# Performance work log

Measured on AMD Instinct MI355X. Metric: run time of the kernel, lower is better.

## Reference

```python
import jax, jax.numpy as jnp
import numpy as np

N_NODES = 50000
N_EDGES = 800000
IN_CH, HID_CH, OUT_CH = 128, 128, 64


def gcn_conv(x, edge_index, edge_weight, W, b, n_nodes):
    """PyG GCNConv: h = D^-1/2 (A + I) D^-1/2 (x @ W) + b, with weighted edges."""
    src, dst = edge_index[0], edge_index[1]
    loop = jnp.arange(n_nodes)
    src_l = jnp.concatenate([src, loop])               # [E+N]
    dst_l = jnp.concatenate([dst, loop])               # [E+N]
    w_l = jnp.concatenate([edge_weight, jnp.ones((n_nodes,), x.dtype)])
    deg = jax.ops.segment_sum(w_l, dst_l, num_segments=n_nodes)  # weighted in-degree incl. self-loop
    dinv = jnp.where(deg > 0, jax.lax.rsqrt(deg), 0.0)
    norm = dinv[src_l] * w_l * dinv[dst_l]             # [E+N]
    h = x @ W                                          # [N, out]
    msg = h[src_l] * norm[:, None]                     # [E+N, out] gather + scale
    out = jax.ops.segment_sum(msg, dst_l, num_segments=n_nodes)  # scatter-add
    return out + b


def setup_inputs() -> dict:
    key = jax.random.key(0)
    k = jax.random.split(key, 8)
    x = jax.random.normal(k[0], (N_NODES, IN_CH), dtype=jnp.float32)
    edge_index = jax.random.randint(k[1], (2, N_EDGES), 0, N_NODES, dtype=jnp.int64)
    edge_weight = jax.random.uniform(k[2], (N_EDGES,), dtype=jnp.float32)
    s1 = 1.0 / np.sqrt(IN_CH)
    s2 = 1.0 / np.sqrt(HID_CH)
    W1 = jax.random.uniform(k[3], (IN_CH, HID_CH), jnp.float32, -s1, s1)
    b1 = jnp.zeros((HID_CH,), jnp.float32)
    W2 = jax.random.uniform(k[4], (HID_CH, OUT_CH), jnp.float32, -s2, s2)
    b2 = jnp.zeros((OUT_CH,), jnp.float32)
    return {"x": x, "edge_index": edge_index, "edge_weight": edge_weight,
            "W1": W1, "b1": b1, "W2": W2, "b2": b2}


def reference(x, edge_index, edge_weight, W1, b1, W2, b2):
    n = x.shape[0]
    h = jax.nn.relu(gcn_conv(x, edge_index, edge_weight, W1, b1, n))
    # dropout(p=0.5) is identity in eval mode
    h = gcn_conv(h, edge_index, edge_weight, W2, b2, n)
    return jax.nn.log_softmax(h, axis=1)
```

## Files before the change

kernel.cpp:

```cpp
#include <hip/hip_runtime.h>
#include <math.h>

static constexpr int CH_IN  = 128;
static constexpr int CH_HID = 128;
static constexpr int CH_OUT = 64;
static constexpr int NBLK1  = 256;

typedef __attribute__((ext_vector_type(8))) short bf16x8;
typedef __attribute__((ext_vector_type(4))) float f32x4;


__device__ __forceinline__ float bf2f(unsigned short u) {
    return __uint_as_float(((unsigned int)u) << 16);
}
__device__ __forceinline__ unsigned short f2bf(float f) {
    unsigned int u = __float_as_uint(f);
    u = (u + 0x7fffu + ((u >> 16) & 1u)) >> 16;
    return (unsigned short)u;
}
__device__ __forceinline__ unsigned int pack2(float lo, float hi) {
    return (unsigned int)f2bf(lo) | ((unsigned int)f2bf(hi) << 16);
}
__device__ __forceinline__ void unpack2(unsigned int u, float& lo, float& hi) {
    lo = __uint_as_float(u << 16);
    hi = __uint_as_float(u & 0xffff0000u);
}
__device__ __forceinline__ unsigned int relu2(unsigned int u) {
    unsigned int m = 0;
    if (!(u & 0x8000u)) m |= 0xffffu;
    if (!(u & 0x80000000u)) m |= 0xffff0000u;
    return u & m;
}

__device__ __forceinline__ void gacc(const uint4* __restrict__ hp, int stride, int ci,
                                     int s, float nm, float* acc) {
    uint4 v = hp[(size_t)s * stride + ci];
    float lo, hi;
    unpack2(v.x, lo, hi); acc[0] = fmaf(lo, nm, acc[0]); acc[1] = fmaf(hi, nm, acc[1]);
    unpack2(v.y, lo, hi); acc[2] = fmaf(lo, nm, acc[2]); acc[3] = fmaf(hi, nm, acc[3]);
    unpack2(v.z, lo, hi); acc[4] = fmaf(lo, nm, acc[4]); acc[5] = fmaf(hi, nm, acc[5]);
    unpack2(v.w, lo, hi); acc[6] = fmaf(lo, nm, acc[6]); acc[7] = fmaf(hi, nm, acc[7]);
}

__device__ __forceinline__ int block_incl_scan_256(int v, int lane, int wid) {
    __shared__ int wtot[4];
    int s = v;
    #pragma unroll
    for (int off = 1; off < 64; off <<= 1) {
        int t = __shfl_up(s, off, 64);
        if (lane >= off) s += t;
    }
    if (lane == 63) wtot[wid] = s;
    __syncthreads();
    int woff = 0;
    for (int j = 0; j < wid; ++j) woff += wtot[j];
    return s + woff;
}


template<int COLS, bool RELU_IN, typename TIN>
__device__ __forceinline__ void gemm_body(const TIN* __restrict__ X,
                                          const unsigned short* __restrict__ Wt,
                                          unsigned short* __restrict__ H, int N, int blk) {
    constexpr int NCT = COLS / 16;
    __shared__ unsigned short As[64 * 136];
    const int tid = threadIdx.x;
    const int lane = tid & 63, wv = tid >> 6;
    const int row0 = blk * 64;

    if constexpr (sizeof(TIN) == 4) {
        #pragma unroll
        for (int j = 0; j < 8; ++j) {
            int f = j * 256 + tid;
            int row = f >> 5, col = (f & 31) * 4;
            float4 v = make_float4(0.f, 0.f, 0.f, 0.f);
            if (row0 + row < N)
                v = *reinterpret_cast<const float4*>((const float*)X + (size_t)(row0 + row) * CH_IN + col);
            uint2 p;
            p.x = pack2(v.x, v.y);
            p.y = pack2(v.z, v.w);
            *reinterpret_cast<uint2*>(&As[row * 136 + col]) = p;
        }
    } else {
        #pragma unroll
        for (int j = 0; j < 4; ++j) {
            int f = j * 256 + tid;
            int row = f >> 4, col = (f & 15) * 8;
            uint4 v = make_uint4(0u, 0u, 0u, 0u);
            if (row0 + row < N) {
                v = *reinterpret_cast<const uint4*>((const unsigned short*)X + (size_t)(row0 + row) * CH_IN + col);
                if (RELU_IN) {
                    v.x = relu2(v.x); v.y = relu2(v.y);
                    v.z = relu2(v.z); v.w = relu2(v.w);
                }
            }
            *reinterpret_cast<uint4*>(&As[row * 136 + col]) = v;
        }
    }
    __syncthreads();

    const int rw0  = wv * 16;
    const int arow = rw0 + (lane & 15);
    const int kgrp = (lane >> 4) * 8;
    f32x4 acc[NCT];
    #pragma unroll
    for (int c = 0; c < NCT; ++c) acc[c] = f32x4{0.f, 0.f, 0.f, 0.f};

    #pragma unroll
    for (int kk = 0; kk < 4; ++kk) {
        bf16x8 af = *reinterpret_cast<const bf16x8*>(&As[arow * 136 + kk * 32 + kgrp]);
        #pragma unroll
        for (int ct = 0; ct < NCT; ++ct) {
            bf16x8 bf = *reinterpret_cast<const bf16x8*>(
                Wt + (size_t)(ct * 16 + (lane & 15)) * 128 + kk * 32 + kgrp);
            acc[ct] = __builtin_amdgcn_mfma_f32_16x16x32_bf16(af, bf, acc[ct], 0, 0, 0);
        }
    }

    const int orow0 = row0 + rw0 + (lane >> 4) * 4;
    const int ocol  = lane & 15;
    #pragma unroll
    for (int ct = 0; ct < NCT; ++ct) {
        #pragma unroll
        for (int r = 0; r < 4; ++r) {
            int row = orow0 + r;
            if (row < N) H[(size_t)row * COLS + ct * 16 + ocol] = f2bf(acc[ct][r]);
        }
    }
}


__global__ void k_count(const int* __restrict__ ei, int* __restrict__ cnt_bk,
                        int E, int nbk, int epb,
                        const float* __restrict__ W1, unsigned short* __restrict__ w1t,
                        const float* __restrict__ W2, unsigned short* __restrict__ w2t) {
    __shared__ int bcnt[256];
    const int tid = threadIdx.x;
    if ((int)blockIdx.x < NBLK1) {
        const int b = blockIdx.x;
        bcnt[tid] = 0;
        __syncthreads();
        const int e0 = b * epb, e1 = min(E, e0 + epb);
        for (int e = e0 + tid; e < e1; e += 256)
            atomicAdd(&bcnt[ei[E + e] >> 8], 1);
        __syncthreads();
        if (tid < nbk) cnt_bk[tid * NBLK1 + b] = bcnt[tid];
    } else {
        int j = (blockIdx.x - NBLK1) * 256 + tid;
        if (j < CH_HID * 128) {
            int c = j >> 7, k = j & 127;
            w1t[(size_t)c * 128 + k] = f2bf(W1[(size_t)k * CH_HID + c]);
            return;
        }
        j -= CH_HID * 128;
        if (j < CH_OUT * 128) {
            int c = j >> 7, k = j & 127;
            w2t[(size_t)c * 128 + k] = f2bf(W2[(size_t)k * CH_OUT + c]);
        }
    }
}


__global__ void k_bscan(const int* __restrict__ cnt_bk, int* __restrict__ off_bk,
                        int* __restrict__ btot) {
    const int k = blockIdx.x, tid = threadIdx.x, lane = tid & 63, wid = tid >> 6;
    int c = cnt_bk[k * NBLK1 + tid];
    int incl = block_incl_scan_256(c, lane, wid);
    off_bk[k * NBLK1 + tid] = incl - c;
    if (tid == 255) btot[k] = incl;
}


__global__ void __launch_bounds__(256) k_fat(
        const float* __restrict__ x, const unsigned short* __restrict__ w1t,
        unsigned short* __restrict__ h1, int N, int nbg,
        const int* __restrict__ ei, const float* __restrict__ w,
        const int* __restrict__ btot, const int* __restrict__ off_bk,
        uint2* __restrict__ ebuck, int E, int nbk, int epb) {
    if ((int)blockIdx.x < nbg) {
        gemm_body<CH_HID, false, float>(x, w1t, h1, N, blockIdx.x);
    } else {
        __shared__ int lcur[256];
        const int b = blockIdx.x - nbg;
        const int tid = threadIdx.x, lane = tid & 63, wid = tid >> 6;
        int v = (tid < nbk) ? btot[tid] : 0;
        int incl = block_incl_scan_256(v, lane, wid);
        if (tid < nbk) lcur[tid] = (incl - v) + off_bk[tid * NBLK1 + b];
        __syncthreads();
        const int e0 = b * epb, e1 = min(E, e0 + epb);
        for (int e = e0 + tid; e < e1; e += 256) {
            unsigned int s = (unsigned int)ei[e];
            unsigned int d = (unsigned int)ei[E + e];
            int pos = atomicAdd(&lcur[d >> 8], 1);
            ebuck[pos] = make_uint2((d << 16) | s, __float_as_uint(w[e]));
        }
    }
}

template<int COLS, bool RELU_IN, typename TIN>
__global__ void __launch_bounds__(256) k_gemm_mfma(const TIN* __restrict__ X,
        const unsigned short* __restrict__ Wt, unsigned short* __restrict__ H, int N) {
    gemm_body<COLS, RELU_IN, TIN>(X, Wt, H, N, blockIdx.x);
}


__global__ void k_csr(const uint2* __restrict__ ebuck, const int* __restrict__ btot,
                      int* __restrict__ rowptr, float* __restrict__ dinv,
                      int2* __restrict__ epack, int N, int nbk) {
    __shared__ int ncnt[256];
    __shared__ float wsm[256];
    __shared__ int ebeg_s, eend_s;
    const int k = blockIdx.x, tid = threadIdx.x, lane = tid & 63, wid = tid >> 6;
    int v = (tid < nbk) ? btot[tid] : 0;
    int incl0 = block_incl_scan_256(v, lane, wid);
    if (tid == k) { ebeg_s = incl0 - v; eend_s = incl0; }
    ncnt[tid] = 0; wsm[tid] = 0.f;
    __syncthreads();
    const int ebeg = ebeg_s, eend = eend_s;
    for (int i = ebeg + tid; i < eend; i += 256) {
        uint2 p = ebuck[i];
        int dl = (p.x >> 16) & 255;
        atomicAdd(&ncnt[dl], 1);
        atomicAdd(&wsm[dl], __uint_as_float(p.y));
    }
    __syncthreads();
    int c = ncnt[tid];
    int incl = block_incl_scan_256(c, lane, wid);
    const int nd = k * 256 + tid;
    if (nd < N) {
        rowptr[nd + 1] = ebeg + incl;
        dinv[nd] = rsqrtf(1.0f + wsm[tid]);
    }
    if (k == 0 && tid == 0) rowptr[0] = 0;
    __syncthreads();
    ncnt[tid] = ebeg + incl - c;
    __syncthreads();
    for (int i = ebeg + tid; i < eend; i += 256) {
        uint2 p = ebuck[i];
        int dl = (p.x >> 16) & 255;
        int pos = atomicAdd(&ncnt[dl], 1);
        epack[pos] = make_int2((int)(p.x & 0xFFFFu), (int)p.y);
    }
}


__global__ void k_agg128(const int* __restrict__ rowptr, const int2* __restrict__ epack,
                         const float* __restrict__ dinv, const unsigned short* __restrict__ h,
                         const float* __restrict__ b, unsigned short* __restrict__ out, int N) {
    const int node = (blockIdx.x * blockDim.x + threadIdx.x) >> 6;
    const int lane = threadIdx.x & 63;
    if (node >= N) return;
    const int beg = rowptr[node], end = rowptr[node + 1];
    const float dd = dinv[node];
    const int g  = lane >> 4;
    const int ci = lane & 15;
    const uint4* hp = (const uint4*)h;

    float acc[8];
    #pragma unroll
    for (int q = 0; q < 8; ++q) acc[q] = 0.f;

    for (int i0 = beg; i0 < end; i0 += 64) {
        const int m = min(64, end - i0);
        int s_l = 0; float nm_l = 0.f;
        if (lane < m) {
            int2 p = epack[i0 + lane];
            s_l = p.x;
            nm_l = __int_as_float(p.y) * dinv[p.x];
        }
        int j = 0;
        for (; j + 16 <= m; j += 16) {
            #pragma unroll
            for (int kk = 0; kk < 4; ++kk) {
                int idx = j + 4 * kk + g;
                int   s  = __shfl(s_l, idx, 64);
                float nm = __shfl(nm_l, idx, 64);
                gacc(hp, 16, ci, s, nm, acc);
            }
        }
        for (; j < m; j += 4) {
            int idx = j + g;
            int   s  = __shfl(s_l, idx, 64);
            float nm = __shfl(nm_l, idx, 64);
            gacc(hp, 16, ci, s, nm, acc);
        }
    }
    #pragma unroll
    for (int q = 0; q < 8; ++q) {
        acc[q] += __shfl_xor(acc[q], 16, 64);
        acc[q] += __shfl_xor(acc[q], 32, 64);
    }
    uint4 hv = hp[(size_t)node * 16 + ci];
    float hn[8];
    unpack2(hv.x, hn[0], hn[1]); unpack2(hv.y, hn[2], hn[3]);
    unpack2(hv.z, hn[4], hn[5]); unpack2(hv.w, hn[6], hn[7]);
    float4 b0 = *reinterpret_cast<const float4*>(b + 8 * ci);
    float4 b1v = *reinterpret_cast<const float4*>(b + 8 * ci + 4);
    const float bb[8] = {b0.x, b0.y, b0.z, b0.w, b1v.x, b1v.y, b1v.z, b1v.w};
    float res[8];
    #pragma unroll
    for (int q = 0; q < 8; ++q)
        res[q] = fmaf(acc[q], dd, fmaf(hn[q], dd * dd, bb[q]));
    if (g == 0) {
        uint4 o;
        o.x = pack2(res[0], res[1]); o.y = pack2(res[2], res[3]);
        o.z = pack2(res[4], res[5]); o.w = pack2(res[6], res[7]);
        ((uint4*)out)[(size_t)node * 16 + ci] = o;
    }
}

__global__ void k_agg64(const int* __restrict__ rowptr, const int2* __restrict__ epack,
                        const float* __restrict__ dinv, const unsigned short* __restrict__ h,
                        const float* __restrict__ b, float* __restrict__ out, int N) {
    const int node = (blockIdx.x * blockDim.x + threadIdx.x) >> 6;
    const int lane = threadIdx.x & 63;
    if (node >= N) return;
    const int beg = rowptr[node], end = rowptr[node + 1];
    const float dd = dinv[node];
    const int g  = lane >> 3;
    const int ci = lane & 7;
    const uint4* hp = (const uint4*)h;

    float acc[8];
    #pragma unroll
    for (int q = 0; q < 8; ++q) acc[q] = 0.f;

    for (int i0 = beg; i0 < end; i0 += 64) {
        const int m = min(64, end - i0);
        int s_l = 0; float nm_l = 0.f;
        if (lane < m) {
            int2 p = epack[i0 + lane];
            s_l = p.x;
            nm_l = __int_as_float(p.y) * dinv[p.x];
        }
        int j = 0;
        for (; j + 32 <= m; j += 32) {
            #pragma unroll
            for (int kk = 0; kk < 4; ++kk) {
                int idx = j + 8 * kk + g;
                int   s  = __shfl(s_l, idx, 64);
                float nm = __shfl(nm_l, idx, 64);
                gacc(hp, 8, ci, s, nm, acc);
            }
        }
        for (; j < m; j += 8) {
            int idx = j + g;
            int   s  = __shfl(s_l, idx, 64);
            float nm = __shfl(nm_l, idx, 64);
            gacc(hp, 8, ci, s, nm, acc);
        }
    }
    #pragma unroll
    for (int q = 0; q < 8; ++q) {
        acc[q] += __shfl_xor(acc[q], 8, 64);
        acc[q] += __shfl_xor(acc[q], 16, 64);
        acc[q] += __shfl_xor(acc[q], 32, 64);
    }
    uint4 hv = hp[(size_t)node * 8 + ci];
    float hn[8];
    unpack2(hv.x, hn[0], hn[1]); unpack2(hv.y, hn[2], hn[3]);
    unpack2(hv.z, hn[4], hn[5]); unpack2(hv.w, hn[6], hn[7]);
    float4 b0 = *reinterpret_cast<const float4*>(b + 8 * ci);
    float4 b1v = *reinterpret_cast<const float4*>(b + 8 * ci + 4);
    const float bb[8] = {b0.x, b0.y, b0.z, b0.w, b1v.x, b1v.y, b1v.z, b1v.w};
    float res[8];
    #pragma unroll
    for (int q = 0; q < 8; ++q)
        res[q] = fmaf(acc[q], dd, fmaf(hn[q], dd * dd, bb[q]));

    float mx = res[0];
    #pragma unroll
    for (int q = 1; q < 8; ++q) mx = fmaxf(mx, res[q]);
    mx = fmaxf(mx, __shfl_xor(mx, 1, 64));
    mx = fmaxf(mx, __shfl_xor(mx, 2, 64));
    mx = fmaxf(mx, __shfl_xor(mx, 4, 64));
    float sm = 0.f;
    #pragma unroll
    for (int q = 0; q < 8; ++q) sm += expf(res[q] - mx);
    sm += __shfl_xor(sm, 1, 64);
    sm += __shfl_xor(sm, 2, 64);
    sm += __shfl_xor(sm, 4, 64);
    float lse = mx + logf(sm);
    if (g == 0) {
        float4 o0 = make_float4(res[0] - lse, res[1] - lse, res[2] - lse, res[3] - lse);
        float4 o1 = make_float4(res[4] - lse, res[5] - lse, res[6] - lse, res[7] - lse);
        *reinterpret_cast<float4*>(out + (size_t)node * 64 + 8 * ci)     = o0;
        *reinterpret_cast<float4*>(out + (size_t)node * 64 + 8 * ci + 4) = o1;
    }
}

extern "C" void kernel_launch(void* const* d_in, const int* in_sizes, int n_in,
                              void* d_out, int out_size, void* d_ws, size_t ws_size,
                              hipStream_t stream) {
    const float* x  = (const float*)d_in[0];
    const int*   ei = (const int*)d_in[1];
    const float* w  = (const float*)d_in[2];
    const float* W1 = (const float*)d_in[3];
    const float* b1 = (const float*)d_in[4];
    const float* W2 = (const float*)d_in[5];
    const float* b2 = (const float*)d_in[6];
    float* out = (float*)d_out;

    const int N = in_sizes[0] / CH_IN;
    const int E = in_sizes[2];
    const int NBK = (N + 255) >> 8;
    const int EPB = (E + NBLK1 - 1) / NBLK1;
    const int WTB = (CH_HID * 128 + CH_OUT * 128 + 255) / 256;

    float* ws0   = (float*)d_ws;
    float* ws    = ws0;
    float* dinv  = ws;               ws += N;
    int*   rowptr= (int*)ws;         ws += (N + 2);
    int*   cnt_bk= (int*)ws;         ws += 256 * NBLK1;
    int*   off_bk= (int*)ws;         ws += 256 * NBLK1;
    int*   btot  = (int*)ws;         ws += 256;
    uint2* ebuck = (uint2*)ws;       ws += (size_t)2 * E;
    int2*  epack = (int2*)ws;        ws += (size_t)2 * E;
    { size_t off = (size_t)(ws - ws0) & 3; if (off) ws += 4 - off; }
    unsigned short* w1t  = (unsigned short*)ws;  ws += (size_t)CH_HID * 128 / 2;
    unsigned short* w2t  = (unsigned short*)ws;  ws += (size_t)CH_OUT * 128 / 2;
    unsigned short* h1   = (unsigned short*)ws;  ws += (size_t)N * CH_HID / 2;
    unsigned short* out1 = (unsigned short*)ws;  ws += (size_t)N * CH_HID / 2;
    unsigned short* h2   = (unsigned short*)ws;  ws += (size_t)N * CH_OUT / 2;

    const int B = 256;

    k_count<<<NBLK1 + WTB, B, 0, stream>>>(ei, cnt_bk, E, NBK, EPB, W1, w1t, W2, w2t);

    k_bscan<<<NBK, 256, 0, stream>>>(cnt_bk, off_bk, btot);

    {
        const int nbg = (N + 63) / 64;
        k_fat<<<nbg + NBLK1, B, 0, stream>>>(x, w1t, h1, N, nbg,
                                             ei, w, btot, off_bk, ebuck, E, NBK, EPB);
    }

    k_csr<<<NBK, 256, 0, stream>>>(ebuck, btot, rowptr, dinv, epack, N, NBK);

    k_agg128<<<(N * 64 + B - 1) / B, B, 0, stream>>>(rowptr, epack, dinv, h1, b1, out1, N);

    k_gemm_mfma<CH_OUT, true, unsigned short><<<(N + 63) / 64, 256, 0, stream>>>(out1, w2t, h2, N);

    k_agg64<<<(N * 64 + B - 1) / B, B, 0, stream>>>(rowptr, epack, dinv, h2, b2, out, N);
}
```

Baseline: 136.9 us.

## Fuse layer-1 aggregation with layer-2 GEMM through shared memory

The layer-1 aggregation kernel and the second bf16 MFMA GEMM are merged into one kernel. Each 512-thread block aggregates 64 nodes, one wave per node in sequence, applies bias and ReLU, stores the rows in LDS, then multiplies them by W2. This removes the out1 intermediate round trip through global memory and one kernel launch. In exchange each wave walks 8 nodes serially and there are fewer blocks, so fewer gathers are in flight at once.

```diff
diff --git a/kernel.cpp b/kernel.cpp
--- a/kernel.cpp
+++ b/kernel.cpp
@@ -24,12 +24,6 @@
 __device__ __forceinline__ void unpack2(unsigned int u, float& lo, float& hi) {
     lo = __uint_as_float(u << 16);
     hi = __uint_as_float(u & 0xffff0000u);
-}
-__device__ __forceinline__ unsigned int relu2(unsigned int u) {
-    unsigned int m = 0;
-    if (!(u & 0x8000u)) m |= 0xffffu;
-    if (!(u & 0x80000000u)) m |= 0xffff0000u;
-    return u & m;
 }
 
 __device__ __forceinline__ void gacc(const uint4* __restrict__ hp, int stride, int ci,
@@ -58,44 +52,26 @@
 }
 
 
-template<int COLS, bool RELU_IN, typename TIN>
-__device__ __forceinline__ void gemm_body(const TIN* __restrict__ X,
-                                          const unsigned short* __restrict__ Wt,
-                                          unsigned short* __restrict__ H, int N, int blk) {
-    constexpr int NCT = COLS / 16;
+__device__ __forceinline__ void gemm128_body(const float* __restrict__ X,
+                                             const unsigned short* __restrict__ Wt,
+                                             unsigned short* __restrict__ H, int N, int blk) {
+    constexpr int NCT = CH_HID / 16;
     __shared__ unsigned short As[64 * 136];
     const int tid = threadIdx.x;
     const int lane = tid & 63, wv = tid >> 6;
     const int row0 = blk * 64;
 
-    if constexpr (sizeof(TIN) == 4) {
-        #pragma unroll
-        for (int j = 0; j < 8; ++j) {
-            int f = j * 256 + tid;
-            int row = f >> 5, col = (f & 31) * 4;
-            float4 v = make_float4(0.f, 0.f, 0.f, 0.f);
-            if (row0 + row < N)
-                v = *reinterpret_cast<const float4*>((const float*)X + (size_t)(row0 + row) * CH_IN + col);
-            uint2 p;
-            p.x = pack2(v.x, v.y);
-            p.y = pack2(v.z, v.w);
-            *reinterpret_cast<uint2*>(&As[row * 136 + col]) = p;
-        }
-    } else {
-        #pragma unroll
-        for (int j = 0; j < 4; ++j) {
-            int f = j * 256 + tid;
-            int row = f >> 4, col = (f & 15) * 8;
-            uint4 v = make_uint4(0u, 0u, 0u, 0u);
-            if (row0 + row < N) {
-                v = *reinterpret_cast<const uint4*>((const unsigned short*)X + (size_t)(row0 + row) * CH_IN + col);
-                if (RELU_IN) {
-                    v.x = relu2(v.x); v.y = relu2(v.y);
-                    v.z = relu2(v.z); v.w = relu2(v.w);
-                }
-            }
-            *reinterpret_cast<uint4*>(&As[row * 136 + col]) = v;
-        }
+    #pragma unroll
+    for (int j = 0; j < 8; ++j) {
+        int f = j * 256 + tid;
+        int row = f >> 5, col = (f & 31) * 4;
+        float4 v = make_float4(0.f, 0.f, 0.f, 0.f);
+        if (row0 + row < N)
+            v = *reinterpret_cast<const float4*>(X + (size_t)(row0 + row) * CH_IN + col);
+        uint2 p;
+        p.x = pack2(v.x, v.y);
+        p.y = pack2(v.z, v.w);
+        *reinterpret_cast<uint2*>(&As[row * 136 + col]) = p;
     }
     __syncthreads();
 
@@ -124,7 +100,7 @@
         #pragma unroll
         for (int r = 0; r < 4; ++r) {
             int row = orow0 + r;
-            if (row < N) H[(size_t)row * COLS + ct * 16 + ocol] = f2bf(acc[ct][r]);
+            if (row < N) H[(size_t)row * CH_HID + ct * 16 + ocol] = f2bf(acc[ct][r]);
         }
     }
 }
@@ -178,7 +154,7 @@
         const int* __restrict__ btot, const int* __restrict__ off_bk,
         uint2* __restrict__ ebuck, int E, int nbk, int epb) {
     if ((int)blockIdx.x < nbg) {
-        gemm_body<CH_HID, false, float>(x, w1t, h1, N, blockIdx.x);
+        gemm128_body(x, w1t, h1, N, blockIdx.x);
     } else {
         __shared__ int lcur[256];
         const int b = blockIdx.x - nbg;
@@ -197,12 +173,6 @@
     }
 }
 
-template<int COLS, bool RELU_IN, typename TIN>
-__global__ void __launch_bounds__(256) k_gemm_mfma(const TIN* __restrict__ X,
-        const unsigned short* __restrict__ Wt, unsigned short* __restrict__ H, int N) {
-    gemm_body<COLS, RELU_IN, TIN>(X, Wt, H, N, blockIdx.x);
-}
-
 
 __global__ void k_csr(const uint2* __restrict__ ebuck, const int* __restrict__ btot,
                       int* __restrict__ rowptr, float* __restrict__ dinv,
@@ -244,70 +214,112 @@
 }
 
 
-__global__ void k_agg128(const int* __restrict__ rowptr, const int2* __restrict__ epack,
-                         const float* __restrict__ dinv, const unsigned short* __restrict__ h,
-                         const float* __restrict__ b, unsigned short* __restrict__ out, int N) {
-    const int node = (blockIdx.x * blockDim.x + threadIdx.x) >> 6;
-    const int lane = threadIdx.x & 63;
-    if (node >= N) return;
-    const int beg = rowptr[node], end = rowptr[node + 1];
-    const float dd = dinv[node];
+__global__ void __launch_bounds__(512) k_aggemm(
+        const int* __restrict__ rowptr, const int2* __restrict__ epack,
+        const float* __restrict__ dinv, const unsigned short* __restrict__ h,
+        const float* __restrict__ b, const unsigned short* __restrict__ w2t,
+        unsigned short* __restrict__ h2, int N) {
+    __shared__ unsigned short As[64 * 136];
+    const int tid = threadIdx.x;
+    const int lane = tid & 63, wv = tid >> 6;
+    const int row0 = blockIdx.x * 64;
     const int g  = lane >> 4;
     const int ci = lane & 15;
     const uint4* hp = (const uint4*)h;
 
-    float acc[8];
-    #pragma unroll
-    for (int q = 0; q < 8; ++q) acc[q] = 0.f;
-
-    for (int i0 = beg; i0 < end; i0 += 64) {
-        const int m = min(64, end - i0);
-        int s_l = 0; float nm_l = 0.f;
-        if (lane < m) {
-            int2 p = epack[i0 + lane];
-            s_l = p.x;
-            nm_l = __int_as_float(p.y) * dinv[p.x];
-        }
-        int j = 0;
-        for (; j + 16 <= m; j += 16) {
+    for (int i = 0; i < 8; ++i) {
+        const int row  = wv * 8 + i;
+        const int node = row0 + row;
+        float acc[8];
+        #pragma unroll
+        for (int q = 0; q < 8; ++q) acc[q] = 0.f;
+        float res[8] = {0.f, 0.f, 0.f, 0.f, 0.f, 0.f, 0.f, 0.f};
+
+        if (node < N) {
+            const int beg = rowptr[node], end = rowptr[node + 1];
+            const float dd = dinv[node];
+            for (int i0 = beg; i0 < end; i0 += 64) {
+                const int m = min(64, end - i0);
+                int s_l = 0; float nm_l = 0.f;
+                if (lane < m) {
+                    int2 p = epack[i0 + lane];
+                    s_l = p.x;
+                    nm_l = __int_as_float(p.y) * dinv[p.x];
+                }
+                int j = 0;
+                for (; j + 16 <= m; j += 16) {
+                    #pragma unroll
+                    for (int kk = 0; kk < 4; ++kk) {
+                        int idx = j + 4 * kk + g;
+                        int   s  = __shfl(s_l, idx, 64);
+                        float nm = __shfl(nm_l, idx, 64);
+                        gacc(hp, 16, ci, s, nm, acc);
+                    }
+                }
+                for (; j < m; j += 4) {
+                    int idx = j + g;
+                    int   s  = __shfl(s_l, idx, 64);
+                    float nm = __shfl(nm_l, idx, 64);
+                    gacc(hp, 16, ci, s, nm, acc);
+                }
+            }
             #pragma unroll
-            for (int kk = 0; kk < 4; ++kk) {
-                int idx = j + 4 * kk + g;
-                int   s  = __shfl(s_l, idx, 64);
-                float nm = __shfl(nm_l, idx, 64);
-                gacc(hp, 16, ci, s, nm, acc);
+            for (int q = 0; q < 8; ++q) {
+                acc[q] += __shfl_xor(acc[q], 16, 64);
+                acc[q] += __shfl_xor(acc[q], 32, 64);
             }
-        }
-        for (; j < m; j += 4) {
-            int idx = j + g;
-            int   s  = __shfl(s_l, idx, 64);
-            float nm = __shfl(nm_l, idx, 64);
-            gacc(hp, 16, ci, s, nm, acc);
-        }
-    }
-    #pragma unroll
-    for (int q = 0; q < 8; ++q) {
-        acc[q] += __shfl_xor(acc[q], 16, 64);
-        acc[q] += __shfl_xor(acc[q], 32, 64);
-    }
-    uint4 hv = hp[(size_t)node * 16 + ci];
-    float hn[8];
-    unpack2(hv.x, hn[0], hn[1]); unpack2(hv.y, hn[2], hn[3]);
-    unpack2(hv.z, hn[4], hn[5]); unpack2(hv.w, hn[6], hn[7]);
-    float4 b0 = *reinterpret_cast<const float4*>(b + 8 * ci);
-    float4 b1v = *reinterpret_cast<const float4*>(b + 8 * ci + 4);
-    const float bb[8] = {b0.x, b0.y, b0.z, b0.w, b1v.x, b1v.y, b1v.z, b1v.w};
-    float res[8];
-    #pragma unroll
-    for (int q = 0; q < 8; ++q)
-        res[q] = fmaf(acc[q], dd, fmaf(hn[q], dd * dd, bb[q]));
-    if (g == 0) {
-        uint4 o;
-        o.x = pack2(res[0], res[1]); o.y = pack2(res[2], res[3]);
-        o.z = pack2(res[4], res[5]); o.w = pack2(res[6], res[7]);
-        ((uint4*)out)[(size_t)node * 16 + ci] = o;
-    }
-}
+            uint4 hv = hp[(size_t)node * 16 + ci];
+            float hn[8];
+            unpack2(hv.x, hn[0], hn[1]); unpack2(hv.y, hn[2], hn[3]);
+            unpack2(hv.z, hn[4], hn[5]); unpack2(hv.w, hn[6], hn[7]);
+            float4 b0 = *reinterpret_cast<const float4*>(b + 8 * ci);
+            float4 b1v = *reinterpret_cast<const float4*>(b + 8 * ci + 4);
+            const float bb[8] = {b0.x, b0.y, b0.z, b0.w, b1v.x, b1v.y, b1v.z, b1v.w};
+            #pragma unroll
+            for (int q = 0; q < 8; ++q)
+                res[q] = fmaxf(fmaf(acc[q], dd, fmaf(hn[q], dd * dd, bb[q])), 0.f);
+        }
+        if (g == 0) {
+            uint4 o;
+            o.x = pack2(res[0], res[1]); o.y = pack2(res[2], res[3]);
+            o.z = pack2(res[4], res[5]); o.w = pack2(res[6], res[7]);
+            *reinterpret_cast<uint4*>(&As[row * 136 + ci * 8]) = o;
+        }
+    }
+    __syncthreads();
+
+    const int rt  = wv >> 1;
+    const int chh = wv & 1;
+    const int arow = rt * 16 + (lane & 15);
+    const int kgrp = (lane >> 4) * 8;
+    f32x4 acc2[2];
+    acc2[0] = f32x4{0.f, 0.f, 0.f, 0.f};
+    acc2[1] = f32x4{0.f, 0.f, 0.f, 0.f};
+
+    #pragma unroll
+    for (int kk = 0; kk < 4; ++kk) {
+        bf16x8 af = *reinterpret_cast<const bf16x8*>(&As[arow * 136 + kk * 32 + kgrp]);
+        #pragma unroll
+        for (int t = 0; t < 2; ++t) {
+            int ct = chh * 2 + t;
+            bf16x8 bf = *reinterpret_cast<const bf16x8*>(
+                w2t + (size_t)(ct * 16 + (lane & 15)) * 128 + kk * 32 + kgrp);
+            acc2[t] = __builtin_amdgcn_mfma_f32_16x16x32_bf16(af, bf, acc2[t], 0, 0, 0);
+        }
+    }
+
+    const int orow0 = row0 + rt * 16 + (lane >> 4) * 4;
+    const int ocol  = lane & 15;
+    #pragma unroll
+    for (int t = 0; t < 2; ++t) {
+        #pragma unroll
+        for (int r = 0; r < 4; ++r) {
+            int row = orow0 + r;
+            if (row < N) h2[(size_t)row * CH_OUT + (chh * 2 + t) * 16 + ocol] = f2bf(acc2[t][r]);
+        }
+    }
+}
+
 
 __global__ void k_agg64(const int* __restrict__ rowptr, const int2* __restrict__ epack,
                         const float* __restrict__ dinv, const unsigned short* __restrict__ h,
@@ -420,7 +432,6 @@
     unsigned short* w1t  = (unsigned short*)ws;  ws += (size_t)CH_HID * 128 / 2;
     unsigned short* w2t  = (unsigned short*)ws;  ws += (size_t)CH_OUT * 128 / 2;
     unsigned short* h1   = (unsigned short*)ws;  ws += (size_t)N * CH_HID / 2;
-    unsigned short* out1 = (unsigned short*)ws;  ws += (size_t)N * CH_HID / 2;
     unsigned short* h2   = (unsigned short*)ws;  ws += (size_t)N * CH_OUT / 2;
 
     const int B = 256;
@@ -437,9 +448,7 @@
 
     k_csr<<<NBK, 256, 0, stream>>>(ebuck, btot, rowptr, dinv, epack, N, NBK);
 
-    k_agg128<<<(N * 64 + B - 1) / B, B, 0, stream>>>(rowptr, epack, dinv, h1, b1, out1, N);
-
-    k_gemm_mfma<CH_OUT, true, unsigned short><<<(N + 63) / 64, 256, 0, stream>>>(out1, w2t, h2, N);
+    k_aggemm<<<(N + 63) / 64, 512, 0, stream>>>(rowptr, epack, dinv, h1, b1, w2t, h2, N);
 
     k_agg64<<<(N * 64 + B - 1) / B, B, 0, stream>>>(rowptr, epack, dinv, h2, b2, out, N);
 }
```

New measurement: 148.4 us. 8.4% more time.

## Quantize first-layer hidden features to int8 with per-row scales for aggregation

Applied to the files above, without the earlier changes.

The first GEMM now writes its output as int8 with a per-row absmax scale instead of bf16. The first aggregation gathers 8 bytes per lane per neighbour instead of 16 and folds the source scale into the edge norm. This halves gather traffic in the dominant sparse aggregation. The cost is a warp shuffle reduction in the GEMM epilogue and a coarser intermediate representation, which risks accuracy loss against the reference. The layer-2 GEMM is split into its own specialized kernel.

```diff
diff --git a/kernel.cpp b/kernel.cpp
--- a/kernel.cpp
+++ b/kernel.cpp
@@ -42,6 +42,20 @@
     unpack2(v.w, lo, hi); acc[6] = fmaf(lo, nm, acc[6]); acc[7] = fmaf(hi, nm, acc[7]);
 }
 
+__device__ __forceinline__ void gacc8(const uint2* __restrict__ hp, int s, int ci,
+                                      float nm, float* acc) {
+    uint2 v = hp[(size_t)s * 16 + ci];
+    int x = (int)v.x, y = (int)v.y;
+    acc[0] = fmaf((float)(char)(x      ), nm, acc[0]);
+    acc[1] = fmaf((float)(char)(x >>  8), nm, acc[1]);
+    acc[2] = fmaf((float)(char)(x >> 16), nm, acc[2]);
+    acc[3] = fmaf((float)(x >> 24),       nm, acc[3]);
+    acc[4] = fmaf((float)(char)(y      ), nm, acc[4]);
+    acc[5] = fmaf((float)(char)(y >>  8), nm, acc[5]);
+    acc[6] = fmaf((float)(char)(y >> 16), nm, acc[6]);
+    acc[7] = fmaf((float)(y >> 24),       nm, acc[7]);
+}
+
 __device__ __forceinline__ int block_incl_scan_256(int v, int lane, int wid) {
     __shared__ int wtot[4];
     int s = v;
@@ -58,44 +72,27 @@
 }
 
 
-template<int COLS, bool RELU_IN, typename TIN>
-__device__ __forceinline__ void gemm_body(const TIN* __restrict__ X,
-                                          const unsigned short* __restrict__ Wt,
-                                          unsigned short* __restrict__ H, int N, int blk) {
-    constexpr int NCT = COLS / 16;
+__device__ __forceinline__ void gemm128q_body(const float* __restrict__ X,
+                                              const unsigned short* __restrict__ Wt,
+                                              signed char* __restrict__ Hq,
+                                              float* __restrict__ scl, int N, int blk) {
+    constexpr int NCT = CH_HID / 16;
     __shared__ unsigned short As[64 * 136];
     const int tid = threadIdx.x;
     const int lane = tid & 63, wv = tid >> 6;
     const int row0 = blk * 64;
 
-    if constexpr (sizeof(TIN) == 4) {
-        #pragma unroll
-        for (int j = 0; j < 8; ++j) {
-            int f = j * 256 + tid;
-            int row = f >> 5, col = (f & 31) * 4;
-            float4 v = make_float4(0.f, 0.f, 0.f, 0.f);
-            if (row0 + row < N)
-                v = *reinterpret_cast<const float4*>((const float*)X + (size_t)(row0 + row) * CH_IN + col);
-            uint2 p;
-            p.x = pack2(v.x, v.y);
-            p.y = pack2(v.z, v.w);
-            *reinterpret_cast<uint2*>(&As[row * 136 + col]) = p;
-        }
-    } else {
-        #pragma unroll
-        for (int j = 0; j < 4; ++j) {
-            int f = j * 256 + tid;
-            int row = f >> 4, col = (f & 15) * 8;
-            uint4 v = make_uint4(0u, 0u, 0u, 0u);
-            if (row0 + row < N) {
-                v = *reinterpret_cast<const uint4*>((const unsigned short*)X + (size_t)(row0 + row) * CH_IN + col);
-                if (RELU_IN) {
-                    v.x = relu2(v.x); v.y = relu2(v.y);
-                    v.z = relu2(v.z); v.w = relu2(v.w);
-                }
-            }
-            *reinterpret_cast<uint4*>(&As[row * 136 + col]) = v;
-        }
+    #pragma unroll
+    for (int j = 0; j < 8; ++j) {
+        int f = j * 256 + tid;
+        int row = f >> 5, col = (f & 31) * 4;
+        float4 v = make_float4(0.f, 0.f, 0.f, 0.f);
+        if (row0 + row < N)
+            v = *reinterpret_cast<const float4*>(X + (size_t)(row0 + row) * CH_IN + col);
+        uint2 p;
+        p.x = pack2(v.x, v.y);
+        p.y = pack2(v.z, v.w);
+        *reinterpret_cast<uint2*>(&As[row * 136 + col]) = p;
     }
     __syncthreads();
 
@@ -120,11 +117,22 @@
     const int orow0 = row0 + rw0 + (lane >> 4) * 4;
     const int ocol  = lane & 15;
     #pragma unroll
-    for (int ct = 0; ct < NCT; ++ct) {
+    for (int r = 0; r < 4; ++r) {
+        float m = 0.f;
         #pragma unroll
-        for (int r = 0; r < 4; ++r) {
-            int row = orow0 + r;
-            if (row < N) H[(size_t)row * COLS + ct * 16 + ocol] = f2bf(acc[ct][r]);
+        for (int ct = 0; ct < NCT; ++ct) m = fmaxf(m, fabsf(acc[ct][r]));
+        m = fmaxf(m, __shfl_xor(m, 1, 64));
+        m = fmaxf(m, __shfl_xor(m, 2, 64));
+        m = fmaxf(m, __shfl_xor(m, 4, 64));
+        m = fmaxf(m, __shfl_xor(m, 8, 64));
+        int row = orow0 + r;
+        float inv = (m > 0.f) ? 127.f / m : 0.f;
+        if (row < N) {
+            if (ocol == 0) scl[row] = (m > 0.f) ? m / 127.f : 0.f;
+            #pragma unroll
+            for (int ct = 0; ct < NCT; ++ct)
+                Hq[(size_t)row * CH_HID + ct * 16 + ocol] =
+                    (signed char)__float2int_rn(acc[ct][r] * inv);
         }
     }
 }
@@ -173,12 +181,12 @@
 
 __global__ void __launch_bounds__(256) k_fat(
         const float* __restrict__ x, const unsigned short* __restrict__ w1t,
-        unsigned short* __restrict__ h1, int N, int nbg,
+        signed char* __restrict__ h1q, float* __restrict__ scl1, int N, int nbg,
         const int* __restrict__ ei, const float* __restrict__ w,
         const int* __restrict__ btot, const int* __restrict__ off_bk,
         uint2* __restrict__ ebuck, int E, int nbk, int epb) {
     if ((int)blockIdx.x < nbg) {
-        gemm_body<CH_HID, false, float>(x, w1t, h1, N, blockIdx.x);
+        gemm128q_body(x, w1t, h1q, scl1, N, blockIdx.x);
     } else {
         __shared__ int lcur[256];
         const int b = blockIdx.x - nbg;
@@ -197,10 +205,57 @@
     }
 }
 
-template<int COLS, bool RELU_IN, typename TIN>
-__global__ void __launch_bounds__(256) k_gemm_mfma(const TIN* __restrict__ X,
+
+__global__ void __launch_bounds__(256) k_gemm2(const unsigned short* __restrict__ X,
         const unsigned short* __restrict__ Wt, unsigned short* __restrict__ H, int N) {
-    gemm_body<COLS, RELU_IN, TIN>(X, Wt, H, N, blockIdx.x);
+    constexpr int COLS = CH_OUT, NCT = COLS / 16;
+    __shared__ unsigned short As[64 * 136];
+    const int tid = threadIdx.x;
+    const int lane = tid & 63, wv = tid >> 6;
+    const int row0 = blockIdx.x * 64;
+
+    #pragma unroll
+    for (int j = 0; j < 4; ++j) {
+        int f = j * 256 + tid;
+        int row = f >> 4, col = (f & 15) * 8;
+        uint4 v = make_uint4(0u, 0u, 0u, 0u);
+        if (row0 + row < N) {
+            v = *reinterpret_cast<const uint4*>(X + (size_t)(row0 + row) * CH_IN + col);
+            v.x = relu2(v.x); v.y = relu2(v.y);
+            v.z = relu2(v.z); v.w = relu2(v.w);
+        }
+        *reinterpret_cast<uint4*>(&As[row * 136 + col]) = v;
+    }
+    __syncthreads();
+
+    const int rw0  = wv * 16;
+    const int arow = rw0 + (lane & 15);
+    const int kgrp = (lane >> 4) * 8;
+    f32x4 acc[NCT];
+    #pragma unroll
+    for (int c = 0; c < NCT; ++c) acc[c] = f32x4{0.f, 0.f, 0.f, 0.f};
+
+    #pragma unroll
+    for (int kk = 0; kk < 4; ++kk) {
+        bf16x8 af = *reinterpret_cast<const bf16x8*>(&As[arow * 136 + kk * 32 + kgrp]);
+        #pragma unroll
+        for (int ct = 0; ct < NCT; ++ct) {
+            bf16x8 bf = *reinterpret_cast<const bf16x8*>(
+                Wt + (size_t)(ct * 16 + (lane & 15)) * 128 + kk * 32 + kgrp);
+            acc[ct] = __builtin_amdgcn_mfma_f32_16x16x32_bf16(af, bf, acc[ct], 0, 0, 0);
+        }
+    }
+
+    const int orow0 = row0 + rw0 + (lane >> 4) * 4;
+    const int ocol  = lane & 15;
+    #pragma unroll
+    for (int ct = 0; ct < NCT; ++ct) {
+        #pragma unroll
+        for (int r = 0; r < 4; ++r) {
+            int row = orow0 + r;
+            if (row < N) H[(size_t)row * COLS + ct * 16 + ocol] = f2bf(acc[ct][r]);
+        }
+    }
 }
 
 
@@ -245,7 +300,8 @@
 
 
 __global__ void k_agg128(const int* __restrict__ rowptr, const int2* __restrict__ epack,
-                         const float* __restrict__ dinv, const unsigned short* __restrict__ h,
+                         const float* __restrict__ dinv, const float* __restrict__ scl,
+                         const signed char* __restrict__ hq,
                          const float* __restrict__ b, unsigned short* __restrict__ out, int N) {
     const int node = (blockIdx.x * blockDim.x + threadIdx.x) >> 6;
     const int lane = threadIdx.x & 63;
@@ -254,7 +310,7 @@
     const float dd = dinv[node];
     const int g  = lane >> 4;
     const int ci = lane & 15;
-    const uint4* hp = (const uint4*)h;
+    const uint2* hp = (const uint2*)hq;
 
     float acc[8];
     #pragma unroll
@@ -266,7 +322,7 @@
         if (lane < m) {
             int2 p = epack[i0 + lane];
             s_l = p.x;
-            nm_l = __int_as_float(p.y) * dinv[p.x];
+            nm_l = __int_as_float(p.y) * dinv[p.x] * scl[p.x];
         }
         int j = 0;
         for (; j + 16 <= m; j += 16) {
@@ -275,14 +331,14 @@
                 int idx = j + 4 * kk + g;
                 int   s  = __shfl(s_l, idx, 64);
                 float nm = __shfl(nm_l, idx, 64);
-                gacc(hp, 16, ci, s, nm, acc);
+                gacc8(hp, s, ci, nm, acc);
             }
         }
         for (; j < m; j += 4) {
             int idx = j + g;
             int   s  = __shfl(s_l, idx, 64);
             float nm = __shfl(nm_l, idx, 64);
-            gacc(hp, 16, ci, s, nm, acc);
+            gacc8(hp, s, ci, nm, acc);
         }
     }
     #pragma unroll
@@ -290,10 +346,14 @@
         acc[q] += __shfl_xor(acc[q], 16, 64);
         acc[q] += __shfl_xor(acc[q], 32, 64);
     }
-    uint4 hv = hp[(size_t)node * 16 + ci];
+    uint2 hv = hp[(size_t)node * 16 + ci];
+    float sc = scl[node];
+    int hx = (int)hv.x, hy = (int)hv.y;
     float hn[8];
-    unpack2(hv.x, hn[0], hn[1]); unpack2(hv.y, hn[2], hn[3]);
-    unpack2(hv.z, hn[4], hn[5]); unpack2(hv.w, hn[6], hn[7]);
+    hn[0] = (float)(char)(hx      ) * sc; hn[1] = (float)(char)(hx >>  8) * sc;
+    hn[2] = (float)(char)(hx >> 16) * sc; hn[3] = (float)(hx >> 24)       * sc;
+    hn[4] = (float)(char)(hy      ) * sc; hn[5] = (float)(char)(hy >>  8) * sc;
+    hn[6] = (float)(char)(hy >> 16) * sc; hn[7] = (float)(hy >> 24)       * sc;
     float4 b0 = *reinterpret_cast<const float4*>(b + 8 * ci);
     float4 b1v = *reinterpret_cast<const float4*>(b + 8 * ci + 4);
     const float bb[8] = {b0.x, b0.y, b0.z, b0.w, b1v.x, b1v.y, b1v.z, b1v.w};
@@ -308,6 +368,7 @@
         ((uint4*)out)[(size_t)node * 16 + ci] = o;
     }
 }
+
 
 __global__ void k_agg64(const int* __restrict__ rowptr, const int2* __restrict__ epack,
                         const float* __restrict__ dinv, const unsigned short* __restrict__ h,
@@ -410,6 +471,7 @@
     float* ws0   = (float*)d_ws;
     float* ws    = ws0;
     float* dinv  = ws;               ws += N;
+    float* scl1  = ws;               ws += N;
     int*   rowptr= (int*)ws;         ws += (N + 2);
     int*   cnt_bk= (int*)ws;         ws += 256 * NBLK1;
     int*   off_bk= (int*)ws;         ws += 256 * NBLK1;
@@ -419,7 +481,7 @@
     { size_t off = (size_t)(ws - ws0) & 3; if (off) ws += 4 - off; }
     unsigned short* w1t  = (unsigned short*)ws;  ws += (size_t)CH_HID * 128 / 2;
     unsigned short* w2t  = (unsigned short*)ws;  ws += (size_t)CH_OUT * 128 / 2;
-    unsigned short* h1   = (unsigned short*)ws;  ws += (size_t)N * CH_HID / 2;
+    signed char*    h1q  = (signed char*)ws;     ws += (size_t)N * CH_HID / 4;
     unsigned short* out1 = (unsigned short*)ws;  ws += (size_t)N * CH_HID / 2;
     unsigned short* h2   = (unsigned short*)ws;  ws += (size_t)N * CH_OUT / 2;
 
@@ -431,15 +493,15 @@
 
     {
         const int nbg = (N + 63) / 64;
-        k_fat<<<nbg + NBLK1, B, 0, stream>>>(x, w1t, h1, N, nbg,
+        k_fat<<<nbg + NBLK1, B, 0, stream>>>(x, w1t, h1q, scl1, N, nbg,
                                              ei, w, btot, off_bk, ebuck, E, NBK, EPB);
     }
 
     k_csr<<<NBK, 256, 0, stream>>>(ebuck, btot, rowptr, dinv, epack, N, NBK);
 
-    k_agg128<<<(N * 64 + B - 1) / B, B, 0, stream>>>(rowptr, epack, dinv, h1, b1, out1, N);
-
-    k_gemm_mfma<CH_OUT, true, unsigned short><<<(N + 63) / 64, 256, 0, stream>>>(out1, w2t, h2, N);
+    k_agg128<<<(N * 64 + B - 1) / B, B, 0, stream>>>(rowptr, epack, dinv, scl1, h1q, b1, out1, N);
+
+    k_gemm2<<<(N + 63) / 64, 256, 0, stream>>>(out1, w2t, h2, N);
 
     k_agg64<<<(N * 64 + B - 1) / B, B, 0, stream>>>(rowptr, epack, dinv, h2, b2, out, N);
 }
```

After: 128.5 us. -6.1%, faster.
